# Kernel optimization log

Hardware: AMD Instinct MI355X
Metric: run time of the kernel (lower is better)

## Reference

```python
import jax, jax.numpy as jnp
import numpy as np

B, C, F = 8192, 2048, 2048


def setup_inputs() -> dict:
    key = jax.random.key(0)
    k1, k2 = jax.random.split(key)
    x = jax.random.normal(k1, (B, F), dtype=jnp.float32)
    means = jax.random.normal(k2, (C, F), dtype=jnp.float32)
    # scalar 'variance' parameter used as a divisor (std); realistic post-update value
    variance = jnp.ones((1,), dtype=jnp.float32)
    return {"x": x, "means": means, "variance": variance}


def reference(x, means, variance):
    # non-deep_nno, eval-mode branch: x = x / std with std = variance param
    xs = x / variance  # [B, F]
    # L2 distance to class means via GEMM cdist: ||a-b|| = sqrt(||a||^2 + ||b||^2 - 2 a.b)
    x2 = jnp.sum(xs * xs, axis=1, keepdims=True)          # [B, 1]
    m2 = jnp.sum(means * means, axis=1)                    # [C]
    cross = jnp.einsum('bf,cf->bc', xs, means)             # [B, C] GEMM
    d2 = jnp.maximum(x2 + m2[None, :] - 2.0 * cross, 0.0)  # clamp fp error
    cumulative_diff = jnp.sqrt(d2)                         # torch.norm(diff, p=2, dim=2)
    exponent = -cumulative_diff
    probs = jax.nn.softmax(exponent, axis=1)
    return (probs, exponent, cumulative_diff)
```

## Files before the change

kernel.cpp:

```cpp
#include <hip/hip_runtime.h>
#include <hip/hip_bf16.h>

constexpr int BB = 8192;
constexpr int CC = 2048;
constexpr int FF = 2048;

typedef __bf16 bf16x8 __attribute__((ext_vector_type(8)));
typedef float  f32x4  __attribute__((ext_vector_type(4)));

typedef __attribute__((address_space(1))) unsigned int gu32;
typedef __attribute__((address_space(3))) unsigned int lu32;

__device__ __forceinline__ void async_copy16(const void* g, void* l) {
    __builtin_amdgcn_global_load_lds(
        (gu32*)(unsigned long long)g,
        (lu32*)(unsigned int)(unsigned long long)l,
        16, 0, 0);
}

__global__ void prep_rows(const float* __restrict__ x,
                          const float* __restrict__ means,
                          unsigned short* __restrict__ xb,
                          unsigned short* __restrict__ mb,
                          float* __restrict__ x2,
                          float* __restrict__ m2,
                          const float* __restrict__ varp) {
    const int blk = blockIdx.x;
    const bool isx = blk < BB;
    const int row = isx ? blk : blk - BB;
    const int t = threadIdx.x;
    const float scale = isx ? (1.0f / varp[0]) : 1.0f;
    const float* in = isx ? x : means;
    unsigned short* outb = isx ? xb : mb;
    const size_t base = (size_t)row * FF + (size_t)t * 8;
    const float4 a = *(const float4*)(in + base);
    const float4 b = *(const float4*)(in + base + 4);
    float v[8] = {a.x * scale, a.y * scale, a.z * scale, a.w * scale,
                  b.x * scale, b.y * scale, b.z * scale, b.w * scale};
    float s = 0.0f;
    bf16x8 h;
#pragma unroll
    for (int i = 0; i < 8; ++i) {
        s += v[i] * v[i];
        h[i] = (__bf16)v[i];
    }
    *(bf16x8*)(outb + base) = h;
#pragma unroll
    for (int off = 32; off > 0; off >>= 1) s += __shfl_down(s, off);
    __shared__ float red[4];
    if ((t & 63) == 0) red[t >> 6] = s;
    __syncthreads();
    if (t == 0) {
        float tot = (red[0] + red[1]) + (red[2] + red[3]);
        if (isx) x2[row] = tot; else m2[row] = tot;
    }
}

__global__ __launch_bounds__(512, 2) void gemm_epi(
    const unsigned short* __restrict__ A,
    const unsigned short* __restrict__ Bm,
    const float* __restrict__ x2,
    const float* __restrict__ m2,
    float* __restrict__ expo,
    float* __restrict__ cum) {
    __shared__ __align__(16) unsigned short As[4][256 * 32];
    __shared__ __align__(16) unsigned short Bs[4][256 * 32];

    const int t = threadIdx.x;
    const int wave = t >> 6, lane = t & 63;
    const int bx = blockIdx.x;
    const int xcd = bx & 7, q = bx >> 3;
    const int bm = xcd * 4 + (q >> 3);
    const int bn = q & 7;
    const int rowA0 = bm * 256, rowB0 = bn * 256;
    const int wm = wave >> 2, wn = wave & 3;

    const int sr = lane >> 2;
    const int sc = ((lane & 3) ^ ((sr >> 1) & 3)) * 8;
    const unsigned short* gA0 = A  + (size_t)(rowA0 +       wave * 16 + sr) * FF + sc;
    const unsigned short* gA1 = A  + (size_t)(rowA0 + 128 + wave * 16 + sr) * FF + sc;
    const unsigned short* gB0 = Bm + (size_t)(rowB0 +       wave * 16 + sr) * FF + sc;
    const unsigned short* gB1 = Bm + (size_t)(rowB0 + 128 + wave * 16 + sr) * FF + sc;
    const int ldsOff = wave * 16 * 32;

    const int rl = lane & 15, kb = lane >> 4;
    const int pcol = (kb ^ ((rl >> 1) & 3)) * 8;
    const int arow = (wm * 128 + rl) * 32 + pcol;
    const int brow = (wn * 64  + rl) * 32 + pcol;

    f32x4 acc[8][4] = {};

    auto STAGE = [&](int slot, int kc) {
        const int ko = kc * 32;
        async_copy16(gA0 + ko, &As[slot][ldsOff]);
        async_copy16(gA1 + ko, &As[slot][128 * 32 + ldsOff]);
        async_copy16(gB0 + ko, &Bs[slot][ldsOff]);
        async_copy16(gB1 + ko, &Bs[slot][128 * 32 + ldsOff]);
    };
    auto COMPUTE = [&](int slot) {
        bf16x8 bfr[4], af[8];
#pragma unroll
        for (int j = 0; j < 4; ++j) bfr[j] = *(const bf16x8*)&Bs[slot][brow + j * 16 * 32];
#pragma unroll
        for (int i = 0; i < 8; ++i) af[i] = *(const bf16x8*)&As[slot][arow + i * 16 * 32];
        __builtin_amdgcn_s_setprio(1);
#pragma unroll
        for (int i = 0; i < 8; ++i)
#pragma unroll
            for (int j = 0; j < 4; ++j)
                acc[i][j] = __builtin_amdgcn_mfma_f32_16x16x32_bf16(af[i], bfr[j], acc[i][j], 0, 0, 0);
        __builtin_amdgcn_s_setprio(0);
    };

    STAGE(0, 0); STAGE(1, 1); STAGE(2, 2);

#pragma unroll 4
    for (int u = 0; u < 60; ++u) {
        asm volatile("s_waitcnt vmcnt(8)" ::: "memory");
        __builtin_amdgcn_s_barrier();
        __builtin_amdgcn_sched_barrier(0);
        STAGE((u + 3) & 3, u + 3);
        COMPUTE(u & 3);
    }
    asm volatile("s_waitcnt vmcnt(8)" ::: "memory");
    __builtin_amdgcn_s_barrier();
    __builtin_amdgcn_sched_barrier(0);
    STAGE(3, 63);
    COMPUTE(0);
    asm volatile("s_waitcnt vmcnt(8)" ::: "memory");
    __builtin_amdgcn_s_barrier();
    __builtin_amdgcn_sched_barrier(0);
    COMPUTE(1);
    asm volatile("s_waitcnt vmcnt(4)" ::: "memory");
    __builtin_amdgcn_s_barrier();
    __builtin_amdgcn_sched_barrier(0);
    COMPUTE(2);
    asm volatile("s_waitcnt vmcnt(0)" ::: "memory");
    __builtin_amdgcn_s_barrier();
    __builtin_amdgcn_sched_barrier(0);
    COMPUTE(3);

    const int ln = lane & 15, lq = lane >> 4;
    const int grow0 = rowA0 + wm * 128 + lq * 4;
    const int gcol0 = rowB0 + wn * 64 + ln;
    float m2v[4];
#pragma unroll
    for (int j = 0; j < 4; ++j) m2v[j] = m2[gcol0 + j * 16];

#pragma unroll
    for (int i = 0; i < 8; ++i) {
        float x2r[4];
#pragma unroll
        for (int r = 0; r < 4; ++r) x2r[r] = x2[grow0 + i * 16 + r];
#pragma unroll
        for (int j = 0; j < 4; ++j)
#pragma unroll
            for (int r = 0; r < 4; ++r) {
                const float d2 = x2r[r] + m2v[j] - 2.0f * acc[i][j][r];
                const float d = sqrtf(fmaxf(d2, 0.0f));
                const size_t idx = (size_t)(grow0 + i * 16 + r) * CC + (gcol0 + j * 16);
                __builtin_nontemporal_store(d, &cum[idx]);
                expo[idx] = -d;
            }
    }
}

__global__ void softmax_rows(const float* __restrict__ e, float* __restrict__ p) {
    const int row = blockIdx.x;
    const int t = threadIdx.x;
    const size_t base = (size_t)row * CC + (size_t)t * 8;
    const float4 a = *(const float4*)(e + base);
    const float4 b = *(const float4*)(e + base + 4);
    float ev[8] = {__expf(a.x), __expf(a.y), __expf(a.z), __expf(a.w),
                   __expf(b.x), __expf(b.y), __expf(b.z), __expf(b.w)};
    float s = 0.0f;
#pragma unroll
    for (int i = 0; i < 8; ++i) s += ev[i];
#pragma unroll
    for (int off = 32; off > 0; off >>= 1) s += __shfl_down(s, off);
    __shared__ float reds[4];
    if ((t & 63) == 0) reds[t >> 6] = s;
    __syncthreads();
    s = (reds[0] + reds[1]) + (reds[2] + reds[3]);
    const float inv = 1.0f / s;

    f32x4 o0 = {ev[0] * inv, ev[1] * inv, ev[2] * inv, ev[3] * inv};
    f32x4 o1 = {ev[4] * inv, ev[5] * inv, ev[6] * inv, ev[7] * inv};
    __builtin_nontemporal_store(o0, (f32x4*)(p + base));
    __builtin_nontemporal_store(o1, (f32x4*)(p + base + 4));
}

extern "C" void kernel_launch(void* const* d_in, const int* in_sizes, int n_in,
                              void* d_out, int out_size, void* d_ws, size_t ws_size,
                              hipStream_t stream) {
    const float* x     = (const float*)d_in[0];
    const float* means = (const float*)d_in[1];
    const float* var   = (const float*)d_in[2];
    float* out = (float*)d_out;

    unsigned short* xb = (unsigned short*)d_ws;
    unsigned short* mb = xb + (size_t)BB * FF;
    float* x2 = (float*)(mb + (size_t)CC * FF);
    float* m2 = x2 + BB;

    float* probs = out;
    float* expo  = out + (size_t)BB * CC;
    float* cum   = expo + (size_t)BB * CC;

    prep_rows<<<BB + CC, 256, 0, stream>>>(x, means, xb, mb, x2, m2, var);
    gemm_epi<<<(BB / 256) * (CC / 256), 512, 0, stream>>>(xb, mb, x2, m2, expo, cum);
    softmax_rows<<<BB, 256, 0, stream>>>(expo, probs);
}
```

Measured before the change: 335.5 us.

## Split GEMM k-step into two MFMA phases with interleaved LDS loads and staging

Each k-chunk of the GEMM main loop now runs as two half-phases. Each phase loads half of the B fragments from LDS, issues half of the global-to-LDS async copies (A in the first phase, B in the second), waits at a barrier, then runs 16 MFMAs. The aim is to interleave memory issue with matrix compute, in the style of ping-pong scheduling, and to hold fewer B fragments in registers at once. The cost is two extra workgroup barriers and lgkmcnt waits per chunk, which could add stalls.

Result: no change. 335.8 us (+0.1%).

```diff
diff --git a/kernel.cpp b/kernel.cpp
--- a/kernel.cpp
+++ b/kernel.cpp
@@ -90,55 +90,70 @@
 
     f32x4 acc[8][4] = {};
 
-    auto STAGE = [&](int slot, int kc) {
+    auto STAGE_A = [&](int slot, int kc) {
         const int ko = kc * 32;
         async_copy16(gA0 + ko, &As[slot][ldsOff]);
         async_copy16(gA1 + ko, &As[slot][128 * 32 + ldsOff]);
+    };
+    auto STAGE_B = [&](int slot, int kc) {
+        const int ko = kc * 32;
         async_copy16(gB0 + ko, &Bs[slot][ldsOff]);
         async_copy16(gB1 + ko, &Bs[slot][128 * 32 + ldsOff]);
     };
-    auto COMPUTE = [&](int slot) {
-        bf16x8 bfr[4], af[8];
-#pragma unroll
-        for (int j = 0; j < 4; ++j) bfr[j] = *(const bf16x8*)&Bs[slot][brow + j * 16 * 32];
+
+    bf16x8 af[8], bf0, bf1, bf2, bf3;
+
+    auto CHUNK = [&](int slot, int nslot, int kc, int vm, bool do_stage) {
+        switch (vm) {
+            case 8: asm volatile("s_waitcnt vmcnt(8)" ::: "memory"); break;
+            case 4: asm volatile("s_waitcnt vmcnt(4)" ::: "memory"); break;
+            default: asm volatile("s_waitcnt vmcnt(0)" ::: "memory"); break;
+        }
+        __builtin_amdgcn_s_barrier();
+        __builtin_amdgcn_sched_barrier(0);
 #pragma unroll
         for (int i = 0; i < 8; ++i) af[i] = *(const bf16x8*)&As[slot][arow + i * 16 * 32];
+        bf0 = *(const bf16x8*)&Bs[slot][brow + 0 * 16 * 32];
+        bf1 = *(const bf16x8*)&Bs[slot][brow + 1 * 16 * 32];
+        if (do_stage) STAGE_A(nslot, kc);
+        __builtin_amdgcn_s_barrier();
+        asm volatile("s_waitcnt lgkmcnt(0)" ::: "memory");
+        __builtin_amdgcn_sched_barrier(0);
         __builtin_amdgcn_s_setprio(1);
 #pragma unroll
-        for (int i = 0; i < 8; ++i)
-#pragma unroll
-            for (int j = 0; j < 4; ++j)
-                acc[i][j] = __builtin_amdgcn_mfma_f32_16x16x32_bf16(af[i], bfr[j], acc[i][j], 0, 0, 0);
+        for (int i = 0; i < 8; ++i) {
+            acc[i][0] = __builtin_amdgcn_mfma_f32_16x16x32_bf16(af[i], bf0, acc[i][0], 0, 0, 0);
+            acc[i][1] = __builtin_amdgcn_mfma_f32_16x16x32_bf16(af[i], bf1, acc[i][1], 0, 0, 0);
+        }
+        __builtin_amdgcn_s_setprio(0);
+        __builtin_amdgcn_s_barrier();
+        __builtin_amdgcn_sched_barrier(0);
+        bf2 = *(const bf16x8*)&Bs[slot][brow + 2 * 16 * 32];
+        bf3 = *(const bf16x8*)&Bs[slot][brow + 3 * 16 * 32];
+        if (do_stage) STAGE_B(nslot, kc);
+        __builtin_amdgcn_s_barrier();
+        asm volatile("s_waitcnt lgkmcnt(0)" ::: "memory");
+        __builtin_amdgcn_sched_barrier(0);
+        __builtin_amdgcn_s_setprio(1);
+#pragma unroll
+        for (int i = 0; i < 8; ++i) {
+            acc[i][2] = __builtin_amdgcn_mfma_f32_16x16x32_bf16(af[i], bf2, acc[i][2], 0, 0, 0);
+            acc[i][3] = __builtin_amdgcn_mfma_f32_16x16x32_bf16(af[i], bf3, acc[i][3], 0, 0, 0);
+        }
         __builtin_amdgcn_s_setprio(0);
     };
 
-    STAGE(0, 0); STAGE(1, 1); STAGE(2, 2);
+    STAGE_A(0, 0); STAGE_B(0, 0);
+    STAGE_A(1, 1); STAGE_B(1, 1);
+    STAGE_A(2, 2); STAGE_B(2, 2);
 
 #pragma unroll 4
-    for (int u = 0; u < 60; ++u) {
-        asm volatile("s_waitcnt vmcnt(8)" ::: "memory");
-        __builtin_amdgcn_s_barrier();
-        __builtin_amdgcn_sched_barrier(0);
-        STAGE((u + 3) & 3, u + 3);
-        COMPUTE(u & 3);
-    }
-    asm volatile("s_waitcnt vmcnt(8)" ::: "memory");
-    __builtin_amdgcn_s_barrier();
-    __builtin_amdgcn_sched_barrier(0);
-    STAGE(3, 63);
-    COMPUTE(0);
-    asm volatile("s_waitcnt vmcnt(8)" ::: "memory");
-    __builtin_amdgcn_s_barrier();
-    __builtin_amdgcn_sched_barrier(0);
-    COMPUTE(1);
-    asm volatile("s_waitcnt vmcnt(4)" ::: "memory");
-    __builtin_amdgcn_s_barrier();
-    __builtin_amdgcn_sched_barrier(0);
-    COMPUTE(2);
-    asm volatile("s_waitcnt vmcnt(0)" ::: "memory");
-    __builtin_amdgcn_s_barrier();
-    __builtin_amdgcn_sched_barrier(0);
-    COMPUTE(3);
+    for (int u = 0; u < 60; ++u)
+        CHUNK(u & 3, (u + 3) & 3, u + 3, 8, true);
+    CHUNK(0, 3, 63, 8, true);
+    CHUNK(1, 0, 0, 8, false);
+    CHUNK(2, 0, 0, 4, false);
+    CHUNK(3, 0, 0, 0, false);
 
     const int ln = lane & 15, lq = lane >> 4;
     const int grow0 = rowA0 + wm * 128 + lq * 4;
```

## Shrink GEMM tile to 256x128 with 3-stage pipeline and higher occupancy

Applied to the files above, without the earlier changes.

The GEMM block tile shrinks from 256x256 to 256x128, so the grid doubles and each wave holds a 4x4 accumulator block instead of 8x4. LDS buffering drops from 4 stages to 3, launch bounds target 4 blocks per CU, and the LDS fragment reads are now issued before the next stage's async copies, with an explicit lgkmcnt wait before the MFMAs. The goal is more resident waves to hide latency and a smaller register and LDS footprint. In exchange, arithmetic intensity per block falls and A is reloaded twice as often from L2.

Measured after the change: 337.4 us. No clear change (+0.6%).

```diff
diff --git a/kernel.cpp b/kernel.cpp
--- a/kernel.cpp
+++ b/kernel.cpp
@@ -56,99 +56,87 @@
     }
 }
 
-__global__ __launch_bounds__(512, 2) void gemm_epi(
+__global__ __launch_bounds__(512, 4) void gemm_epi(
     const unsigned short* __restrict__ A,
     const unsigned short* __restrict__ Bm,
     const float* __restrict__ x2,
     const float* __restrict__ m2,
     float* __restrict__ expo,
     float* __restrict__ cum) {
-    __shared__ __align__(16) unsigned short As[4][256 * 32];
-    __shared__ __align__(16) unsigned short Bs[4][256 * 32];
+    __shared__ __align__(16) unsigned short As[3][256 * 32];
+    __shared__ __align__(16) unsigned short Bs[3][128 * 32];
 
     const int t = threadIdx.x;
     const int wave = t >> 6, lane = t & 63;
     const int bx = blockIdx.x;
-    const int xcd = bx & 7, q = bx >> 3;
-    const int bm = xcd * 4 + (q >> 3);
-    const int bn = q & 7;
-    const int rowA0 = bm * 256, rowB0 = bn * 256;
-    const int wm = wave >> 2, wn = wave & 3;
+    const int xcd = bx & 7, lid = bx >> 3;
+    const int bm = xcd * 4 + (lid >> 4);
+    const int bn = lid & 15;
+    const int rowA0 = bm * 256, colB0 = bn * 128;
+    const int wm = wave >> 1, wn = wave & 1;
 
     const int sr = lane >> 2;
     const int sc = ((lane & 3) ^ ((sr >> 1) & 3)) * 8;
     const unsigned short* gA0 = A  + (size_t)(rowA0 +       wave * 16 + sr) * FF + sc;
     const unsigned short* gA1 = A  + (size_t)(rowA0 + 128 + wave * 16 + sr) * FF + sc;
-    const unsigned short* gB0 = Bm + (size_t)(rowB0 +       wave * 16 + sr) * FF + sc;
-    const unsigned short* gB1 = Bm + (size_t)(rowB0 + 128 + wave * 16 + sr) * FF + sc;
+    const unsigned short* gB0 = Bm + (size_t)(colB0 +       wave * 16 + sr) * FF + sc;
     const int ldsOff = wave * 16 * 32;
 
     const int rl = lane & 15, kb = lane >> 4;
     const int pcol = (kb ^ ((rl >> 1) & 3)) * 8;
-    const int arow = (wm * 128 + rl) * 32 + pcol;
-    const int brow = (wn * 64  + rl) * 32 + pcol;
-
-    f32x4 acc[8][4] = {};
+    const int arow = (wm * 64 + rl) * 32 + pcol;
+    const int brow = (wn * 64 + rl) * 32 + pcol;
+
+    f32x4 acc[4][4] = {};
 
     auto STAGE = [&](int slot, int kc) {
         const int ko = kc * 32;
         async_copy16(gA0 + ko, &As[slot][ldsOff]);
         async_copy16(gA1 + ko, &As[slot][128 * 32 + ldsOff]);
         async_copy16(gB0 + ko, &Bs[slot][ldsOff]);
-        async_copy16(gB1 + ko, &Bs[slot][128 * 32 + ldsOff]);
     };
-    auto COMPUTE = [&](int slot) {
-        bf16x8 bfr[4], af[8];
+
+    auto CHUNK = [&](int slot, int nslot, int kc, int vm, bool do_stage) {
+        if (vm == 3) asm volatile("s_waitcnt vmcnt(3)" ::: "memory");
+        else         asm volatile("s_waitcnt vmcnt(0)" ::: "memory");
+        __builtin_amdgcn_s_barrier();
+        __builtin_amdgcn_sched_barrier(0);
+        bf16x8 af[4], bfr[4];
+#pragma unroll
+        for (int i = 0; i < 4; ++i) af[i] = *(const bf16x8*)&As[slot][arow + i * 16 * 32];
 #pragma unroll
         for (int j = 0; j < 4; ++j) bfr[j] = *(const bf16x8*)&Bs[slot][brow + j * 16 * 32];
-#pragma unroll
-        for (int i = 0; i < 8; ++i) af[i] = *(const bf16x8*)&As[slot][arow + i * 16 * 32];
+        if (do_stage) STAGE(nslot, kc);
+        asm volatile("s_waitcnt lgkmcnt(0)" ::: "memory");
+        __builtin_amdgcn_sched_barrier(0);
         __builtin_amdgcn_s_setprio(1);
 #pragma unroll
-        for (int i = 0; i < 8; ++i)
+        for (int i = 0; i < 4; ++i)
 #pragma unroll
             for (int j = 0; j < 4; ++j)
                 acc[i][j] = __builtin_amdgcn_mfma_f32_16x16x32_bf16(af[i], bfr[j], acc[i][j], 0, 0, 0);
         __builtin_amdgcn_s_setprio(0);
     };
 
-    STAGE(0, 0); STAGE(1, 1); STAGE(2, 2);
-
-#pragma unroll 4
-    for (int u = 0; u < 60; ++u) {
-        asm volatile("s_waitcnt vmcnt(8)" ::: "memory");
-        __builtin_amdgcn_s_barrier();
-        __builtin_amdgcn_sched_barrier(0);
-        STAGE((u + 3) & 3, u + 3);
-        COMPUTE(u & 3);
-    }
-    asm volatile("s_waitcnt vmcnt(8)" ::: "memory");
-    __builtin_amdgcn_s_barrier();
-    __builtin_amdgcn_sched_barrier(0);
-    STAGE(3, 63);
-    COMPUTE(0);
-    asm volatile("s_waitcnt vmcnt(8)" ::: "memory");
-    __builtin_amdgcn_s_barrier();
-    __builtin_amdgcn_sched_barrier(0);
-    COMPUTE(1);
-    asm volatile("s_waitcnt vmcnt(4)" ::: "memory");
-    __builtin_amdgcn_s_barrier();
-    __builtin_amdgcn_sched_barrier(0);
-    COMPUTE(2);
-    asm volatile("s_waitcnt vmcnt(0)" ::: "memory");
-    __builtin_amdgcn_s_barrier();
-    __builtin_amdgcn_sched_barrier(0);
-    COMPUTE(3);
+    STAGE(0, 0); STAGE(1, 1);
+
+#pragma unroll 3
+    for (int u = 0; u < 60; ++u)
+        CHUNK(u % 3, (u + 2) % 3, u + 2, 3, true);
+    CHUNK(0, 2, 62, 3, true);
+    CHUNK(1, 0, 63, 3, true);
+    CHUNK(2, 0, 0, 3, false);
+    CHUNK(0, 0, 0, 0, false);
 
     const int ln = lane & 15, lq = lane >> 4;
-    const int grow0 = rowA0 + wm * 128 + lq * 4;
-    const int gcol0 = rowB0 + wn * 64 + ln;
+    const int grow0 = rowA0 + wm * 64 + lq * 4;
+    const int gcol0 = colB0 + wn * 64 + ln;
     float m2v[4];
 #pragma unroll
     for (int j = 0; j < 4; ++j) m2v[j] = m2[gcol0 + j * 16];
 
 #pragma unroll
-    for (int i = 0; i < 8; ++i) {
+    for (int i = 0; i < 4; ++i) {
         float x2r[4];
 #pragma unroll
         for (int r = 0; r < 4; ++r) x2r[r] = x2[grow0 + i * 16 + r];
@@ -208,6 +196,6 @@
     float* cum   = expo + (size_t)BB * CC;
 
     prep_rows<<<BB + CC, 256, 0, stream>>>(x, means, xb, mb, x2, m2, var);
-    gemm_epi<<<(BB / 256) * (CC / 256), 512, 0, stream>>>(xb, mb, x2, m2, expo, cum);
+    gemm_epi<<<(BB / 256) * (CC / 128), 512, 0, stream>>>(xb, mb, x2, m2, expo, cum);
     softmax_rows<<<BB, 256, 0, stream>>>(expo, probs);
 }
```
